# Performance work log

Hardware: AMD Instinct MI355X
Metric: run time of the kernel (lower is better)

## Reference

```python
import jax, jax.numpy as jnp
import numpy as np

NEG = 0.2  # LeakyReLU slope

def lrelu(x):
    return jnp.where(x >= 0, x, NEG * x)

def conv2d(x, w, pad):
    return jax.lax.conv_general_dilated(x, w, (1, 1), [(pad, pad), (pad, pad)],
                                        dimension_numbers=('NCHW', 'OIHW', 'NCHW'))

def maxpool2(x):
    return jax.lax.reduce_window(x, -jnp.inf, jax.lax.max, (1, 1, 2, 2), (1, 1, 2, 2), 'VALID')

def batchnorm(x, g, b, eps=1e-5):
    m = jnp.mean(x, axis=(0, 2, 3), keepdims=True)
    v = jnp.var(x, axis=(0, 2, 3), keepdims=True)
    return (x - m) / jnp.sqrt(v + eps) * g[None, :, None, None] + b[None, :, None, None]

def features(x, cw1, bg1, bb1, cw2, bg2, bb2, cw3, bg3, bb3, cw4, bg4, bb4):
    x = maxpool2(lrelu(batchnorm(conv2d(x, cw1, 1), bg1, bb1)))
    x = maxpool2(lrelu(batchnorm(conv2d(x, cw2, 1), bg2, bb2)))
    x = lrelu(batchnorm(conv2d(x, cw3, 1), bg3, bb3))
    x = lrelu(batchnorm(conv2d(x, cw4, 1), bg4, bb4))
    return x  # [B,64,16,16]

def mhsa(x, wq, bq, wk, bk, wv, bv, rel_h, rel_w, ln_g, ln_b, heads=4):
    B, C, W, H = x.shape
    d, hw = C // heads, W * H
    def proj(w, b):
        return (jnp.einsum('oc,bchw->bohw', w, x) + b[None, :, None, None]).reshape(B, heads, d, hw)
    q, k, v = proj(wq, bq), proj(wk, bk), proj(wv, bv)
    cc = jnp.einsum('bhdi,bhdj->bhij', q, k)                 # content-content
    pos = (rel_h + rel_w).reshape(heads, d, hw)              # relative position bias
    cp = jnp.einsum('hdi,bhdj->bhij', pos, q)                # content-position
    attn = jax.nn.softmax(cc + cp, axis=-1)
    out = jnp.einsum('bhdj,bhij->bhdi', v, attn).reshape(B, C, W, H)
    m = jnp.mean(out, axis=(1, 2, 3), keepdims=True)
    va = jnp.var(out, axis=(1, 2, 3), keepdims=True)
    out = (out - m) / jnp.sqrt(va + 1e-5) * ln_g[None] + ln_b[None]
    return out + x

def cbam(x, cw1, cb1, cw2, cb2, sw, sb):
    avg, mx = jnp.mean(x, axis=(2, 3)), jnp.max(x, axis=(2, 3))
    def exc(f):
        return jnp.einsum('oc,bc->bo', cw2, jax.nn.relu(jnp.einsum('oc,bc->bo', cw1, f) + cb1)) + cb2
    x = jax.nn.sigmoid(exc(avg) + exc(mx))[:, :, None, None] * x
    sf = jnp.stack([jnp.mean(x, axis=1), jnp.max(x, axis=1)], axis=1)  # [B,2,H,W]
    sa = jax.nn.sigmoid(conv2d(sf, sw, 3) + sb[None, :, None, None])
    return sa * x

def sa_module(x, mh, cb):
    return mhsa(x, *mh) + cbam(x, *cb) + x

def setup_inputs() -> dict:
    key = jax.random.key(0)
    ks = jax.random.split(key, 24)
    rn = lambda k, s, sc=1.0: jax.random.normal(k, s, dtype=jnp.float32) * sc
    inp = {
        'input1': rn(ks[0], (64, 1, 64, 64)),
        'input2': rn(ks[1], (5, 5, 1, 64, 64)),
        'conv1_w': rn(ks[2], (64, 1, 3, 3), 0.3),
        'bn1_g': jnp.ones(64), 'bn1_b': jnp.zeros(64),
        'conv2_w': rn(ks[3], (64, 64, 3, 3), 0.05),
        'bn2_g': jnp.ones(64), 'bn2_b': jnp.zeros(64),
        'conv3_w': rn(ks[4], (64, 64, 3, 3), 0.05),
        'bn3_g': jnp.ones(64), 'bn3_b': jnp.zeros(64),
        'conv4_w': rn(ks[5], (64, 64, 3, 3), 0.05),
        'bn4_g': jnp.ones(64), 'bn4_b': jnp.zeros(64),
        'wq': rn(ks[6], (64, 64), 0.12), 'bq': rn(ks[7], (64,), 0.01),
        'wk': rn(ks[8], (64, 64), 0.12), 'bk': rn(ks[9], (64,), 0.01),
        'wv': rn(ks[10], (64, 64), 0.12), 'bv': rn(ks[11], (64,), 0.01),
        'rel_h': rn(ks[12], (1, 4, 16, 1, 16)),
        'rel_w': rn(ks[13], (1, 4, 16, 16, 1)),
        'ln_g': jnp.ones((64, 16, 16)), 'ln_b': jnp.zeros((64, 16, 16)),
        'ca_w1': rn(ks[14], (4, 64), 0.15), 'ca_b1': jnp.zeros(4),
        'ca_w2': rn(ks[15], (64, 4), 0.15), 'ca_b2': jnp.zeros(64),
        'sa_w': rn(ks[16], (1, 2, 7, 7), 0.1), 'sa_b': jnp.zeros(1),
        'cls_w': rn(ks[17], (256,), 0.05),
    }
    return inp

def reference(input1, input2, conv1_w, bn1_g, bn1_b, conv2_w, bn2_g, bn2_b,
              conv3_w, bn3_g, bn3_b, conv4_w, bn4_g, bn4_b,
              wq, bq, wk, bk, wv, bv, rel_h, rel_w, ln_g, ln_b,
              ca_w1, ca_b1, ca_w2, ca_b2, sa_w, sa_b, cls_w):
    fa = (conv1_w, bn1_g, bn1_b, conv2_w, bn2_g, bn2_b, conv3_w, bn3_g, bn3_b, conv4_w, bn4_g, bn4_b)
    mh = (wq, bq, wk, bk, wv, bv, rel_h, rel_w, ln_g, ln_b)
    cb = (ca_w1, ca_b1, ca_w2, ca_b2, sa_w, sa_b)
    q = sa_module(features(input1, *fa), mh, cb)                      # [B,64,16,16]
    S = jax.vmap(lambda imgs: sa_module(features(imgs, *fa), mh, cb))(input2)  # [ncls,shot,64,16,16]
    ncls, shot = input2.shape[0], input2.shape[1]
    B, C, Hh, Ww = q.shape
    hw = Hh * Ww
    # per-class covariance over channels (CovaBlock.cal_covariance)
    X = S.transpose(0, 2, 1, 3, 4).reshape(ncls, C, shot * hw)
    Xc = X - jnp.mean(X, axis=2, keepdims=True)
    cov = jnp.einsum('ncm,ndm->ncd', Xc, Xc) / (hw * shot - 1)        # [ncls,C,C]
    # query similarity: diag(q^T Cov q) done as fused quadratic form
    Q = q.reshape(B, C, hw)
    Qn = Q / jnp.linalg.norm(Q, axis=2, keepdims=True)
    sim = jnp.einsum('bci,jcd,bdi->bji', Qn, cov, Qn)                 # [B,ncls,hw]
    # classifier: LeakyReLU -> Dropout(eval=identity) -> Conv1d(k=hw, stride=hw, no bias)
    out = jnp.einsum('bjk,k->bj', lrelu(sim), cls_w)
    return out
```

## Files before the change

### kernel.cpp

```cpp
#include <hip/hip_runtime.h>
#include <hip/hip_bf16.h>

__device__ __forceinline__ float lrelu(float x){ return x >= 0.f ? x : 0.2f*x; }
__device__ __forceinline__ float sigm(float x){ return 1.f/(1.f+__expf(-x)); }

typedef short short8 __attribute__((ext_vector_type(8)));
typedef float f32x16 __attribute__((ext_vector_type(16)));

static constexpr size_t OFF_X0    = 0;
static constexpr size_t OFF_POS   = 475712;
static constexpr size_t OFF_WQT   = 492096;
static constexpr size_t OFF_STATS = 504384;
static constexpr size_t OFF_P1    = 507456;
static constexpr size_t OFF_P2    = 6340160;
static constexpr size_t OFF_RES   = 10714688;
static constexpr size_t OFF_MU    = 12172864;
static constexpr size_t OFF_COV   = 12173184;
static constexpr size_t OFF_SIM   = 12193664;
static constexpr size_t OFF_R1    = 12275584;
static constexpr size_t OFF_C2    = OFF_R1;
static constexpr size_t OFF_ATP   = OFF_R1;
static constexpr size_t OFF_C3    = OFF_R1 + 5832704;
static constexpr size_t OFF_C4    = OFF_R1 + 8749056;
static constexpr size_t OFF_CKV   = OFF_R1 + 10207232;
static constexpr size_t OFF_MHRAW = OFF_R1 + 14581760;
static constexpr size_t OFF_QN    = OFF_R1 + 17543680;
static constexpr size_t OFF_WH    = OFF_R1 + 21737984;
static constexpr size_t OFF_WL    = OFF_WH + 18432;

__device__ __forceinline__ int bn_group(int img){ return (img < 64) ? 0 : (1 + (img-64)/5); }

__device__ __forceinline__ void bn_ab(const float* __restrict__ sums, int g, int c, float n,
                                      float gw, float bw, float& a, float& b)
{
    const float sum = sums[(g*64+c)*2], ss = sums[(g*64+c)*2+1];
    const float m = sum/n;
    const float var = fmaxf(ss/n - m*m, 0.f);
    const float istd = 1.f/sqrtf(var + 1e-5f);
    a = gw*istd;
    b = bw - m*a;
}

__global__ __launch_bounds__(256) void prep_k(const float* __restrict__ in1, const float* __restrict__ in2,
        const float* __restrict__ relh, const float* __restrict__ relw,
        const float* __restrict__ wq, const float* __restrict__ wk, const float* __restrict__ wv,
        const float* __restrict__ cw2,
        float* __restrict__ ws)
{
    int idx = blockIdx.x*256 + threadIdx.x;
    if (idx < 364544) { ws[OFF_X0+idx] = (idx < 262144 ? in1[idx] : in2[idx-262144]); return; }
    idx -= 364544;
    if (idx < 16384) {
        const int h = idx>>12, r = idx&4095, i = r>>4, d = r&15;
        ws[OFF_POS+idx] = relh[h*256 + d*16 + (i&15)] + relw[h*256 + d*16 + (i>>4)];
        return;
    }
    idx -= 16384;
    if (idx < 12288) {
        const int s = idx/4096, r = idx%4096, c = r>>6, o = r&63;
        const float* wp = (s==0)?wq:((s==1)?wk:wv);
        ws[OFF_WQT+idx] = wp[o*64 + c];
        return;
    }
    idx -= 12288;
    if (idx < 3072) { ws[OFF_STATS+idx] = 0.f; return; }
    idx -= 3072;
    if (idx < 20480) { ws[OFF_COV+idx] = 0.f; return; }
    idx -= 20480;
    if (idx < 36864) {
        const int och = idx/576, r = idx%576, cin = r/9, k9 = r%9;
        const float v = cw2[idx];
        __hip_bfloat16 hb = __float2bfloat16(v);
        const float hv = __bfloat162float(hb);
        __hip_bfloat16 lb = __float2bfloat16(v - hv);
        unsigned short* WH = (unsigned short*)(ws + OFF_WH);
        unsigned short* WL = (unsigned short*)(ws + OFF_WL);
        const int d = k9*4096 + och*64 + cin;
        WH[d] = *(unsigned short*)&hb;
        WL[d] = *(unsigned short*)&lb;
    }
}

template<int H, int W, int CIN, int CH, int OCB, int PT, bool STORE, bool INBN>
__global__ __launch_bounds__(256) void conv3x3_k(const float* __restrict__ in,
                                                 const float* __restrict__ wt,
                                                 float* __restrict__ out,
                                                 float* __restrict__ bnsum,
                                                 const float* __restrict__ isums,
                                                 const float* __restrict__ igw,
                                                 const float* __restrict__ ibw,
                                                 int ihw)
{
    constexpr int P = W + 1;
    constexpr int PLANE = H * P;
    constexpr int HW = H * W;
    constexpr int PASSES = HW / (256 * PT);
    constexpr int NLD = CH * HW / 256;
    __shared__ float lds[CH * PLANE];
    __shared__ float redS[OCB*4], redQ[OCB*4];
    __shared__ float abA[64], abB[64];
    const int img = blockIdx.x;
    const int och0 = blockIdx.y * OCB;
    const int t = threadIdx.x;

    if constexpr (INBN) {
        if (t < CIN) {
            const int gi = bn_group(img);
            const float nin = (float)(((gi==0)?64:5) * ihw);
            float a, b;
            bn_ab(isums, gi, t, nin, igw[t], ibw[t], a, b);
            abA[t]=a; abB[t]=b;
        }
        __syncthreads();
    }

    float acc[PASSES][OCB][PT];
#pragma unroll
    for (int a=0;a<PASSES;a++)
#pragma unroll
      for (int o=0;o<OCB;o++)
#pragma unroll
        for (int p=0;p<PT;p++) acc[a][o][p]=0.f;

    for (int idx = t; idx < CH*HW; idx += 256) {
        const int c = idx / HW, p = idx % HW;
        float v = in[((size_t)img*CIN + c)*HW + p];
        if constexpr (INBN) v = lrelu(abA[c]*v + abB[c]);
        lds[c*PLANE + (p/W)*P + (p%W)] = v;
    }
    __syncthreads();

    for (int cc0 = 0; cc0 < CIN; cc0 += CH) {
        float pre[(CIN > CH) ? NLD : 1];
        if constexpr (CIN > CH) {
            if (cc0 + CH < CIN) {
#pragma unroll
                for (int j=0;j<NLD;j++){
                    const int idx = j*256 + t;
                    const int c = idx / HW, p = idx % HW;
                    pre[j] = in[((size_t)img*CIN + cc0 + CH + c)*HW + p];
                }
            }
        }
        for (int c = 0; c < CH; ++c) {
            float wr[OCB][9];
#pragma unroll
            for (int o=0;o<OCB;o++)
#pragma unroll
              for (int k=0;k<9;k++)
                wr[o][k] = wt[((size_t)(och0+o)*CIN + (cc0+c))*9 + k];
            const float* Lc = lds + c*PLANE;
#pragma unroll
            for (int ps=0; ps<PASSES; ++ps) {
                const int px0 = (ps*256 + t)*PT;
                const int y = px0 / W, x0 = px0 % W;
#pragma unroll
                for (int ky=0; ky<3; ++ky) {
                    const int yy = y + ky - 1;
                    if (yy >= 0 && yy < H) {
                        const float* Lr = Lc + yy*P;
                        float r[PT+2];
                        r[0] = (x0 > 0) ? Lr[x0-1] : 0.f;
#pragma unroll
                        for (int k2=0;k2<PT;k2++) r[k2+1] = Lr[x0+k2];
                        r[PT+1] = (x0+PT < W) ? Lr[x0+PT] : 0.f;
#pragma unroll
                        for (int p=0;p<PT;p++)
#pragma unroll
                          for (int kx=0;kx<3;kx++) {
                              const float v = r[p+kx];
#pragma unroll
                              for (int o=0;o<OCB;o++)
                                  acc[ps][o][p] += v * wr[o][ky*3+kx];
                          }
                    }
                }
            }
        }
        if constexpr (CIN > CH) {
            if (cc0 + CH < CIN) {
                __syncthreads();
#pragma unroll
                for (int j=0;j<NLD;j++){
                    const int idx = j*256 + t;
                    const int c = idx / HW, p = idx % HW;
                    float v = pre[j];
                    if constexpr (INBN) v = lrelu(abA[cc0+CH+c]*v + abB[cc0+CH+c]);
                    lds[c*PLANE + (p/W)*P + (p%W)] = v;
                }
                __syncthreads();
            }
        }
    }
    if constexpr (STORE) {
#pragma unroll
        for (int ps=0; ps<PASSES; ++ps) {
            const int px0 = (ps*256 + t)*PT;
#pragma unroll
            for (int o=0;o<OCB;o++)
#pragma unroll
              for (int p=0;p<PT;p++)
                out[((size_t)img*64 + och0+o)*HW + px0 + p] = acc[ps][o][p];
        }
    }
    const int g = bn_group(img);
    const int wv = t >> 6;
#pragma unroll
    for (int o=0;o<OCB;o++){
        float s=0.f, ss=0.f;
#pragma unroll
        for (int ps=0;ps<PASSES;ps++)
#pragma unroll
          for (int p=0;p<PT;p++){ const float v=acc[ps][o][p]; s+=v; ss+=v*v; }
#pragma unroll
        for (int off=32; off>0; off>>=1){ s += __shfl_xor(s, off); ss += __shfl_xor(ss, off); }
        if ((t&63)==0){ redS[o*4+wv]=s; redQ[o*4+wv]=ss; }
    }
    __syncthreads();
    if (t < OCB*2){
        const int o = t>>1, metric = t&1;
        const float v = metric ? (redQ[o*4]+redQ[o*4+1]+redQ[o*4+2]+redQ[o*4+3])
                               : (redS[o*4]+redS[o*4+1]+redS[o*4+2]+redS[o*4+3]);
        atomicAdd(&bnsum[(g*64 + och0+o)*2 + metric], v);
    }
}

__global__ __launch_bounds__(256) void conv2mfma_k(const float* __restrict__ p1,
        const unsigned short* __restrict__ whi, const unsigned short* __restrict__ wlo,
        float* __restrict__ c2)
{
    __shared__ __align__(16) unsigned short Bx[6*34*72];
    const int img = blockIdx.x, rowblk = blockIdx.y;
    const int t = threadIdx.x;

    for (int i=t; i<6*2*72; i+=256){
        const int ly = i/144, r2 = i%144, xs = r2/72, c = r2%72;
        Bx[(ly*34 + xs*33)*72 + c] = 0;
    }
    unsigned int lo_pack[24];
    const int y0 = rowblk*4 - 1;
    {
        int it = 0;
        for (int lin=t; lin<12288; lin+=256, ++it){
            const int c = lin/192, r = lin%192, ly = r>>5, x = r&31;
            const int y = y0 + ly;
            float v = 0.f;
            if (y>=0 && y<32) v = p1[((size_t)img*64 + c)*1024 + y*32 + x];
            __hip_bfloat16 hb = __float2bfloat16(v);
            const float hv = __bfloat162float(hb);
            __hip_bfloat16 lb = __float2bfloat16(v - hv);
            Bx[(ly*34 + x + 1)*72 + c] = *(unsigned short*)&hb;
            const unsigned int lu = *(unsigned short*)&lb;
            if (it & 1) lo_pack[it>>1] |= (lu<<16); else lo_pack[it>>1] = lu;
        }
    }
    __syncthreads();

    const int lane = t & 63, wv = t >> 6;
    const int mt = wv & 1, ntp = wv >> 1;
    const int m = lane & 31, kg = lane >> 5;
    const int nt0 = ntp*2, nt1 = nt0 + 1;

    f32x16 acc0, acc1;
#pragma unroll
    for (int r=0;r<16;r++){ acc0[r]=0.f; acc1[r]=0.f; }

    for (int ky=0; ky<3; ky++){
      for (int kx=0; kx<3; kx++){
        const int s = ky*3 + kx;
        const unsigned short* wh = whi + ((s*64 + mt*32 + m)<<6) + kg*8;
        const unsigned short* wl = wlo + ((s*64 + mt*32 + m)<<6) + kg*8;
        const int b0 = ((nt0+ky)*34 + m + kx)*72 + kg*8;
        const int b1 = ((nt1+ky)*34 + m + kx)*72 + kg*8;
        short8 ah[4], al[4], bh0[4], bh1[4];
#pragma unroll
        for (int ch=0; ch<4; ch++){
            ah[ch]  = *(const short8*)(wh + ch*16);
            al[ch]  = *(const short8*)(wl + ch*16);
            bh0[ch] = *(const short8*)(Bx + b0 + ch*16);
            bh1[ch] = *(const short8*)(Bx + b1 + ch*16);
        }
#pragma unroll
        for (int ch=0; ch<4; ch++){
            acc0 = __builtin_amdgcn_mfma_f32_32x32x16_bf16(ah[ch], bh0[ch], acc0, 0,0,0);
            acc1 = __builtin_amdgcn_mfma_f32_32x32x16_bf16(ah[ch], bh1[ch], acc1, 0,0,0);
        }
#pragma unroll
        for (int ch=0; ch<4; ch++){
            acc0 = __builtin_amdgcn_mfma_f32_32x32x16_bf16(al[ch], bh0[ch], acc0, 0,0,0);
            acc1 = __builtin_amdgcn_mfma_f32_32x32x16_bf16(al[ch], bh1[ch], acc1, 0,0,0);
        }
      }
    }
    __syncthreads();
    {
        int it = 0;
        for (int lin=t; lin<12288; lin+=256, ++it){
            const int c = lin/192, r = lin%192, ly = r>>5, x = r&31;
            const unsigned int lu = (it&1) ? (lo_pack[it>>1]>>16) : (lo_pack[it>>1]&0xffffu);
            Bx[(ly*34 + x + 1)*72 + c] = (unsigned short)lu;
        }
    }
    __syncthreads();
    for (int ky=0; ky<3; ky++){
      for (int kx=0; kx<3; kx++){
        const int s = ky*3 + kx;
        const unsigned short* wh = whi + ((s*64 + mt*32 + m)<<6) + kg*8;
        const int b0 = ((nt0+ky)*34 + m + kx)*72 + kg*8;
        const int b1 = ((nt1+ky)*34 + m + kx)*72 + kg*8;
#pragma unroll
        for (int ch=0; ch<4; ch++){
            const short8 ah  = *(const short8*)(wh + ch*16);
            const short8 bl0 = *(const short8*)(Bx + b0 + ch*16);
            const short8 bl1 = *(const short8*)(Bx + b1 + ch*16);
            acc0 = __builtin_amdgcn_mfma_f32_32x32x16_bf16(ah, bl0, acc0, 0,0,0);
            acc1 = __builtin_amdgcn_mfma_f32_32x32x16_bf16(ah, bl1, acc1, 0,0,0);
        }
      }
    }
    const int px0 = (rowblk*4 + nt0)*32 + m;
    const int px1 = (rowblk*4 + nt1)*32 + m;
#pragma unroll
    for (int r=0; r<16; r++){
        const int och = mt*32 + (r&3) + 8*(r>>2) + 4*kg;
        c2[((size_t)img*64 + och)*1024 + px0] = acc0[r];
        c2[((size_t)img*64 + och)*1024 + px1] = acc1[r];
    }
}

__global__ __launch_bounds__(256) void bnstats2_k(const float* __restrict__ in, float* __restrict__ sums)
{
    __shared__ float rs[4], rq[4];
    const int img = blockIdx.x, c = blockIdx.y, t = threadIdx.x;
    const float4 v = ((const float4*)(in + ((size_t)img*64 + c)*1024))[t];
    float s = v.x+v.y+v.z+v.w;
    float q = v.x*v.x+v.y*v.y+v.z*v.z+v.w*v.w;
#pragma unroll
    for (int off=32; off>0; off>>=1){ s += __shfl_xor(s, off); q += __shfl_xor(q, off); }
    if ((t&63)==0){ rs[t>>6]=s; rq[t>>6]=q; }
    __syncthreads();
    if (t==0){
        const int g = bn_group(img);
        atomicAdd(&sums[(g*64+c)*2],   rs[0]+rs[1]+rs[2]+rs[3]);
        atomicAdd(&sums[(g*64+c)*2+1], rq[0]+rq[1]+rq[2]+rq[3]);
    }
}

__global__ __launch_bounds__(256) void bnpoolconv1_k(const float* __restrict__ x0,
        const float* __restrict__ cw, const float* __restrict__ sums,
        const float* __restrict__ gw, const float* __restrict__ bw,
        float* __restrict__ out)
{
    __shared__ float xl[64*65];
    const int img = blockIdx.x, och = blockIdx.y, t = threadIdx.x;
    const float* xp = x0 + (size_t)img*4096;
    for (int idx=t; idx<4096; idx+=256) xl[(idx>>6)*65 + (idx&63)] = xp[idx];
    float w[9];
#pragma unroll
    for (int k=0;k<9;k++) w[k] = cw[och*9+k];
    const int g = bn_group(img);
    const float n = (float)(((g==0)?64:5) * 4096);
    float a, b;
    bn_ab(sums, g, och, n, gw[och], bw[och], a, b);
    __syncthreads();
    const int oy = t>>3, ox0 = (t&7)*4;
    float r[4][10];
#pragma unroll
    for (int rr=0; rr<4; ++rr){
        const int yy = 2*oy-1+rr;
#pragma unroll
        for (int cc=0; cc<10; ++cc){
            const int xx = 2*ox0-1+cc;
            r[rr][cc] = (yy>=0 && yy<64 && xx>=0 && xx<64) ? xl[yy*65+xx] : 0.f;
        }
    }
    float4 res;
    float* rp = (float*)&res;
#pragma unroll
    for (int p=0;p<4;p++){
        float best = -1e30f;
#pragma unroll
        for (int sy=0; sy<2; ++sy)
#pragma unroll
          for (int sx=0; sx<2; ++sx){
            float s=0.f;
#pragma unroll
            for (int ky=0;ky<3;ky++)
#pragma unroll
              for (int kx=0;kx<3;kx++)
                s += r[sy+ky][2*p+sx+kx]*w[ky*3+kx];
            best = fmaxf(best, lrelu(a*s+b));
          }
        rp[p] = best;
    }
    *(float4*)(out + ((size_t)img*64+och)*1024 + oy*32 + ox0) = res;
}

template<int H, int W>
__global__ __launch_bounds__(256) void bnpool_k(const float* __restrict__ in, const float* __restrict__ sums,
                                 const float* __restrict__ gw, const float* __restrict__ bw,
                                 float* __restrict__ out)
{
    const int img = blockIdx.x, c = blockIdx.y, t = threadIdx.x;
    const int g = bn_group(img);
    const float n = (float)(((g==0)?64:5) * H * W);
    float a, b;
    bn_ab(sums, g, c, n, gw[c], bw[c], a, b);
    constexpr int W2=W/2, HW=H*W, N2=(H/2)*W2;
    const float* pl = in + ((size_t)img*64 + c)*HW;
    float* po = out + ((size_t)img*64 + c)*N2;
    for (int opx=t; opx<N2; opx+=256) {
        const int oy=opx/W2, ox=opx%W2;
        const float* q = pl + (2*oy)*W + 2*ox;
        const float v0=lrelu(a*q[0]+b), v1=lrelu(a*q[1]+b), v2=lrelu(a*q[W]+b), v3=lrelu(a*q[W+1]+b);
        po[opx] = fmaxf(fmaxf(v0,v1),fmaxf(v2,v3));
    }
}

__global__ __launch_bounds__(256) void proj_k(const float* __restrict__ c4, const float* __restrict__ wT,
               const float* __restrict__ bq, const float* __restrict__ bk, const float* __restrict__ bv,
               const float* __restrict__ sums4, const float* __restrict__ gw4, const float* __restrict__ bw4,
               float* __restrict__ ckv)
{
    __shared__ float xl[64*256];
    const int img = blockIdx.x, s = blockIdx.y, t = threadIdx.x;
    const int gi = bn_group(img);
    const float nin = (float)(((gi==0)?64:5) * 256);
    {
        const float4* in4 = (const float4*)(c4 + (size_t)img*16384);
        float4* xl4 = (float4*)xl;
        for (int i=t; i<4096; i+=256){
            float4 v = in4[i];
            const int c = i>>6;
            float a, b;
            bn_ab(sums4, gi, c, nin, gw4[c], bw4[c], a, b);
            v.x=lrelu(a*v.x+b); v.y=lrelu(a*v.y+b); v.z=lrelu(a*v.z+b); v.w=lrelu(a*v.w+b);
            xl4[i] = v;
        }
    }
    const float* bias = (s==0)?bq:((s==1)?bk:bv);
    const int sofs = (s==0)?16:((s==1)?0:32);
    const float* wp = wT + s*4096;
    const int o0 = (t>>4)*4, i0 = (t&15)*16;
    const int h = o0>>4, d0 = o0&15;
    __syncthreads();
    float acc[4][16];
    float b0[4];
#pragma unroll
    for (int o=0;o<4;o++) b0[o]=bias[o0+o];
#pragma unroll
    for (int o=0;o<4;o++)
#pragma unroll
      for (int i=0;i<16;i++) acc[o][i]=b0[o];
    for (int c=0;c<64;c++){
        const float4 w4 = *(const float4*)(wp + c*64 + o0);
        const float* xr = xl + c*256 + i0;
#pragma unroll
        for (int k=0;k<4;k++){
            const float4 x4 = *(const float4*)(xr + 4*k);
            acc[0][4*k+0]+=w4.x*x4.x; acc[0][4*k+1]+=w4.x*x4.y; acc[0][4*k+2]+=w4.x*x4.z; acc[0][4*k+3]+=w4.x*x4.w;
            acc[1][4*k+0]+=w4.y*x4.x; acc[1][4*k+1]+=w4.y*x4.y; acc[1][4*k+2]+=w4.y*x4.z; acc[1][4*k+3]+=w4.y*x4.w;
            acc[2][4*k+0]+=w4.z*x4.x; acc[2][4*k+1]+=w4.z*x4.y; acc[2][4*k+2]+=w4.z*x4.z; acc[2][4*k+3]+=w4.z*x4.w;
            acc[3][4*k+0]+=w4.w*x4.x; acc[3][4*k+1]+=w4.w*x4.y; acc[3][4*k+2]+=w4.w*x4.z; acc[3][4*k+3]+=w4.w*x4.w;
        }
    }
#pragma unroll
    for (int ii=0;ii<16;ii++){
        const float4 v = make_float4(acc[0][ii],acc[1][ii],acc[2][ii],acc[3][ii]);
        *(float4*)(ckv + (((size_t)img*4 + h)*256 + i0+ii)*48 + sofs + d0) = v;
    }
}

__global__ __launch_bounds__(256) void attnp_k(const float* __restrict__ ckv, const float* __restrict__ pos,
                               float* __restrict__ part)
{
    const int img = blockIdx.x, h = blockIdx.y, jc = blockIdx.z, i = threadIdx.x;
    const size_t jb = (((size_t)img*4 + h)*256)*48;
    float areg[32];
    {
        const float* myrow = ckv + jb + (size_t)i*48;
#pragma unroll
        for (int k=0;k<4;k++) *(float4*)&areg[4*k]    = *(const float4*)(myrow + 16 + 4*k);
#pragma unroll
        for (int k=0;k<4;k++) *(float4*)&areg[16+4*k] = *(const float4*)(pos + h*4096 + i*16 + 4*k);
    }
    float mrun = -1e30f, l = 0.f;
    float accv[16];
#pragma unroll
    for (int d=0;d<16;d++) accv[d]=0.f;

    const int jend = jc*64 + 64;
    for (int j0=jc*64; j0<jend; j0+=2){
        const float* r0 = ckv + jb + (size_t)j0*48;
        const float* r1 = r0 + 48;
        float s0a=0.f, s0b=0.f, s1a=0.f, s1b=0.f;
#pragma unroll
        for (int dd=0; dd<16; ++dd){
            s0a += areg[2*dd]  *r0[2*dd];
            s0b += areg[2*dd+1]*r0[2*dd+1];
            s1a += areg[2*dd]  *r1[2*dd];
            s1b += areg[2*dd+1]*r1[2*dd+1];
        }
        const float s0 = s0a+s0b, s1 = s1a+s1b;
        const float mnew = fmaxf(mrun, fmaxf(s0,s1));
        const float al = __expf(mrun - mnew);
        const float e0 = __expf(s0 - mnew), e1 = __expf(s1 - mnew);
        mrun = mnew;
        l = l*al + e0 + e1;
        const float* v0 = r0 + 32;
        const float* v1 = r1 + 32;
#pragma unroll
        for (int d=0;d<16;d++) accv[d] = accv[d]*al + e0*v0[d] + e1*v1[d];
    }
    float* pp = part + ((((size_t)img*4 + h)*4 + jc)*18)*256;
    pp[i]       = mrun;
    pp[256 + i] = l;
#pragma unroll
    for (int d=0;d<16;d++) pp[(2+d)*256 + i] = accv[d];
}

__global__ __launch_bounds__(256) void attnm_k(const float* __restrict__ part, float* __restrict__ mhraw)
{
    const int img = blockIdx.x, h = blockIdx.y, i = threadIdx.x;
    const float* pb = part + (((size_t)img*4 + h)*4*18)*256;
    float mc[4], lc[4];
#pragma unroll
    for (int c=0;c<4;c++){ mc[c] = pb[c*4608 + i]; lc[c] = pb[c*4608 + 256 + i]; }
    const float ms = fmaxf(fmaxf(mc[0],mc[1]), fmaxf(mc[2],mc[3]));
    float wgt[4]; float ls = 0.f;
#pragma unroll
    for (int c=0;c<4;c++){ wgt[c] = __expf(mc[c]-ms); ls += wgt[c]*lc[c]; }
    const float rl = 1.f/ls;
#pragma unroll
    for (int d=0;d<16;d++){
        float v = 0.f;
#pragma unroll
        for (int c=0;c<4;c++) v += wgt[c]*pb[c*4608 + (2+d)*256 + i];
        mhraw[((size_t)img*64 + h*16 + d)*256 + i] = v*rl;
    }
}

__global__ __launch_bounds__(256) void post_k(const float* __restrict__ mhraw,
        const float* __restrict__ lng, const float* __restrict__ lnb,
        const float* __restrict__ c4,
        const float* __restrict__ sums4, const float* __restrict__ gw4, const float* __restrict__ bw4,
        const float* __restrict__ w1, const float* __restrict__ b1,
        const float* __restrict__ w2, const float* __restrict__ b2,
        const float* __restrict__ sw, const float* __restrict__ sb,
        float* __restrict__ res)
{
    __shared__ float r1[256], r2[256];
    __shared__ float favg[64], fmx[64], z1s[8], ca[64];
    __shared__ float sf[512];
    __shared__ float wl[98];
    __shared__ float mh_s[2];
    __shared__ float aA[64], aB[64];
    __shared__ float sa_l[256];
    const int img = blockIdx.x, t = threadIdx.x;
    const float* mb  = mhraw + (size_t)img*16384;
    const float* fbr = c4    + (size_t)img*16384;

    if (t<64){
        const int gi = bn_group(img);
        const float nin = (float)(((gi==0)?64:5) * 256);
        float a, b;
        bn_ab(sums4, gi, t, nin, gw4[t], bw4[t], a, b);
        aA[t]=a; aB[t]=b;
    }
    if (t<98) wl[t] = sw[t];

    {
        const float4* mb4 = (const float4*)mb;
        float s=0.f, ss=0.f;
        for (int i=t; i<4096; i+=256){
            const float4 v = mb4[i];
            s  += v.x+v.y+v.z+v.w;
            ss += v.x*v.x+v.y*v.y+v.z*v.z+v.w*v.w;
        }
        r1[t]=s; r2[t]=ss; __syncthreads();
        for (int st=128;st>0;st>>=1){ if(t<st){r1[t]+=r1[t+st]; r2[t]+=r2[t+st];} __syncthreads(); }
        if (t==0){
            const float m = r1[0]/16384.f;
            const float var = fmaxf(r2[0]/16384.f - m*m, 0.f);
            mh_s[0]=m; mh_s[1]=1.f/sqrtf(var+1e-5f);
        }
    }
    {
        const int c = t>>2, part = t&3;
        const float a = aA[c], b = aB[c];
        const float4* p4 = (const float4*)(fbr + c*256 + part*64);
        float s=0.f, mx=-1e30f;
        for (int k=0;k<16;k++){
            const float4 v = p4[k];
            const float f0=lrelu(a*v.x+b), f1=lrelu(a*v.y+b), f2=lrelu(a*v.z+b), f3=lrelu(a*v.w+b);
            s += f0+f1+f2+f3;
            mx = fmaxf(mx, fmaxf(fmaxf(f0,f1),fmaxf(f2,f3)));
        }
        __syncthreads();
        r1[t]=s; r2[t]=mx;
        __syncthreads();
        if (t<64){
            favg[t] = (r1[t*4]+r1[t*4+1]+r1[t*4+2]+r1[t*4+3])/256.f;
            fmx[t]  = fmaxf(fmaxf(r2[t*4],r2[t*4+1]),fmaxf(r2[t*4+2],r2[t*4+3]));
        }
    }
    __syncthreads();
    if (t<8){
        const int which = t>>2, o = t&3;
        const float* f = which? fmx : favg;
        float z = b1[o];
        for (int c=0;c<64;c++) z += w1[o*64+c]*f[c];
        z1s[t] = fmaxf(z, 0.f);
    }
    __syncthreads();
    if (t<64){
        float z = 2.f*b2[t];
#pragma unroll
        for (int k=0;k<4;k++) z += w2[t*4+k]*(z1s[k]+z1s[4+k]);
        ca[t] = sigm(z);
    }
    __syncthreads();
    {
        float s=0.f, mx=-1e30f;
        for (int c=0;c<64;c++){
            const float fv = lrelu(aA[c]*fbr[c*256+t] + aB[c]);
            const float v = ca[c]*fv;
            s += v; mx = fmaxf(mx, v);
        }
        sf[t]     = s/64.f;
        sf[256+t] = mx;
    }
    __syncthreads();
    {
        float sacc = sb[0];
        const int y = t>>4, x = t&15;
        for (int ch=0; ch<2; ++ch)
          for (int ky=0; ky<7; ++ky){
            const int yy = y+ky-3;
            if (yy<0||yy>=16) continue;
            for (int kx=0; kx<7; ++kx){
                const int xx = x+kx-3;
                if (xx<0||xx>=16) continue;
                sacc += sf[ch*256 + yy*16 + xx]*wl[ch*49 + ky*7 + kx];
            }
          }
        sa_l[t] = sigm(sacc);
    }
    __syncthreads();
    {
        const int q = t & 63;
        const int cb = t >> 6;
        const float m = mh_s[0], istd = mh_s[1];
        const float4* mb4 = (const float4*)mb;
        const float4* fb4 = (const float4*)fbr;
        const float4* lg4 = (const float4*)lng;
        const float4* lb4 = (const float4*)lnb;
        float4* res4 = (float4*)(res + (size_t)img*16384);
        const float sa0=sa_l[4*q], sa1=sa_l[4*q+1], sa2=sa_l[4*q+2], sa3=sa_l[4*q+3];
#pragma unroll 4
        for (int cc=0; cc<16; ++cc){
            const int c = cb*16 + cc;
            const int i4 = c*64 + q;
            const float4 mv = mb4[i4], fv = fb4[i4], gv = lg4[i4], bv = lb4[i4];
            const float a = aA[c], b = aB[c], cf = ca[c];
            float4 r;
            r.x = (mv.x-m)*istd*gv.x + bv.x + lrelu(a*fv.x+b)*(2.f + sa0*cf);
            r.y = (mv.y-m)*istd*gv.y + bv.y + lrelu(a*fv.y+b)*(2.f + sa1*cf);
            r.z = (mv.z-m)*istd*gv.z + bv.z + lrelu(a*fv.z+b)*(2.f + sa2*cf);
            r.w = (mv.w-m)*istd*gv.w + bv.w + lrelu(a*fv.w+b)*(2.f + sa3*cf);
            res4[i4] = r;
        }
    }
}

__global__ __launch_bounds__(256) void covmu_k(const float* __restrict__ res, float* __restrict__ mu)
{
    __shared__ float r1[256];
    const int n = blockIdx.x, c = blockIdx.y, t = threadIdx.x;
    float s=0.f;
    for (int sh=0; sh<5; ++sh)
        s += res[((size_t)(64 + n*5 + sh)*64 + c)*256 + t];
    r1[t]=s; __syncthreads();
    for (int st=128;st>0;st>>=1){ if(t<st) r1[t]+=r1[t+st]; __syncthreads(); }
    if (t==0) mu[n*64+c] = r1[0]/1280.f;
}

__global__ __launch_bounds__(256) void cov_k(const float* __restrict__ res, const float* __restrict__ mu,
                                             float* __restrict__ cov)
{
    __shared__ float Xl[64*129];
    const int n = blockIdx.x, by = blockIdx.y, sh = blockIdx.z, t = threadIdx.x;
    const int c = by*16 + (t>>4);
    const int d0 = (t&15)*4;
    float acc[4] = {0.f,0.f,0.f,0.f};
    for (int half=0; half<2; ++half){
        __syncthreads();
        for (int idx=t; idx<8192; idx+=256){
            const int ch = idx>>7, p = idx&127;
            Xl[ch*129+p] = res[((size_t)(64+n*5+sh)*64 + ch)*256 + half*128 + p] - mu[n*64+ch];
        }
        __syncthreads();
        for (int p=0;p<128;p++){
            const float xc = Xl[c*129+p];
#pragma unroll
            for (int k=0;k<4;k++) acc[k] += xc*Xl[(d0+k)*129+p];
        }
    }
#pragma unroll
    for (int k=0;k<4;k++) atomicAdd(&cov[((size_t)n*64 + c)*64 + d0+k], acc[k]*(1.f/1279.f));
}

__global__ __launch_bounds__(64) void qn_k(const float* __restrict__ res, float* __restrict__ qn)
{
    const int b = blockIdx.x, c = blockIdx.y, t = threadIdx.x;
    const size_t base = ((size_t)b*64 + c)*256;
    const float4 v = *(const float4*)(res + base + t*4);
    float ss = v.x*v.x + v.y*v.y + v.z*v.z + v.w*v.w;
#pragma unroll
    for (int off=32; off>0; off>>=1) ss += __shfl_xor(ss, off);
    const float inv = 1.f/sqrtf(ss);
    float4 o; o.x=v.x*inv; o.y=v.y*inv; o.z=v.z*inv; o.w=v.w*inv;
    *(float4*)(qn + base + t*4) = o;
}

__global__ __launch_bounds__(256) void sim_k(const float* __restrict__ qn, const float* __restrict__ cov,
                                             float* __restrict__ sim)
{
    __shared__ float covj[64*65];
    __shared__ float Vl[64*68];
    __shared__ float simred[320];
    const int b = blockIdx.x, iq = blockIdx.y, t = threadIdx.x;
    const int i0g = iq*64;
    for (int idx=t; idx<4096; idx+=256){
        const int c = idx>>6, il = idx&63;
        Vl[c*68+il] = qn[((size_t)b*64+c)*256 + i0g + il];
    }
    for (int idx=t; idx<320; idx+=256) simred[idx]=0.f;
    const int c0 = (t>>4)*4, i0 = (t&15)*4;
    for (int j=0;j<5;j++){
        __syncthreads();
        for (int idx=t; idx<4096; idx+=256)
            covj[(idx>>6)*65 + (idx&63)] = cov[(size_t)j*4096 + idx];
        __syncthreads();
        float pt[4][4];
#pragma unroll
        for (int a=0;a<4;a++)
#pragma unroll
          for (int bb=0;bb<4;bb++) pt[a][bb]=0.f;
        for (int d=0; d<64; ++d){
            const float4 vv = *(const float4*)&Vl[d*68 + i0];
            float cw[4];
#pragma unroll
            for (int cc=0;cc<4;cc++) cw[cc] = covj[(c0+cc)*65 + d];
#pragma unroll
            for (int cc=0;cc<4;cc++){
                pt[cc][0] += cw[cc]*vv.x;
                pt[cc][1] += cw[cc]*vv.y;
                pt[cc][2] += cw[cc]*vv.z;
                pt[cc][3] += cw[cc]*vv.w;
            }
        }
#pragma unroll
        for (int ii=0;ii<4;ii++){
            float s = 0.f;
#pragma unroll
            for (int cc=0;cc<4;cc++) s += pt[cc][ii]*Vl[(c0+cc)*68 + i0+ii];
            atomicAdd(&simred[j*64 + i0 + ii], s);
        }
    }
    __syncthreads();
    for (int idx=t; idx<320; idx+=256){
        const int j = idx>>6, il = idx&63;
        sim[((size_t)b*5 + j)*256 + i0g + il] = simred[idx];
    }
}

__global__ __launch_bounds__(256) void cls_k(const float* __restrict__ sim, const float* __restrict__ cw,
                                             float* __restrict__ out)
{
    __shared__ float red[256];
    const int b = blockIdx.x, t = threadIdx.x;
    const float w = cw[t];
    for (int j=0;j<5;j++){
        const float v = sim[((size_t)b*5 + j)*256 + t];
        red[t] = lrelu(v)*w;
        __syncthreads();
        for (int st=128;st>0;st>>=1){ if(t<st) red[t]+=red[t+st]; __syncthreads(); }
        if (t==0) out[b*5+j] = red[0];
        __syncthreads();
    }
}

extern "C" void kernel_launch(void* const* d_in, const int* in_sizes, int n_in,
                              void* d_out, int out_size, void* d_ws, size_t ws_size,
                              hipStream_t stream)
{
    const float* IN[31];
    for (int i=0;i<31;i++) IN[i] = (const float*)d_in[i];
    float* W = (float*)d_ws;
    float* OUT = (float*)d_out;
    const unsigned short* WHp = (const unsigned short*)(W + OFF_WH);
    const unsigned short* WLp = (const unsigned short*)(W + OFF_WL);

    prep_k<<<1772,256,0,stream>>>(IN[0],IN[1],IN[20],IN[21],IN[14],IN[16],IN[18],IN[5],W);

    conv3x3_k<64,64,1,1,4,4,false,false><<<dim3(89,16),256,0,stream>>>(W+OFF_X0, IN[2], nullptr, W+OFF_STATS, nullptr,nullptr,nullptr,0);
    bnpoolconv1_k<<<dim3(89,64),256,0,stream>>>(W+OFF_X0, IN[2], W+OFF_STATS, IN[3], IN[4], W+OFF_P1);

    conv2mfma_k<<<dim3(89,8),256,0,stream>>>(W+OFF_P1, WHp, WLp, W+OFF_C2);
    bnstats2_k<<<dim3(89,64),256,0,stream>>>(W+OFF_C2, W+OFF_STATS+768);
    bnpool_k<32,32><<<dim3(89,64),256,0,stream>>>(W+OFF_C2, W+OFF_STATS+768, IN[6], IN[7], W+OFF_P2);

    conv3x3_k<16,16,64,16,8,1,true,false><<<dim3(89,8),256,0,stream>>>(W+OFF_P2, IN[8], W+OFF_C3, W+OFF_STATS+1536, nullptr,nullptr,nullptr,0);

    conv3x3_k<16,16,64,16,8,1,true,true><<<dim3(89,8),256,0,stream>>>(W+OFF_C3, IN[11], W+OFF_C4, W+OFF_STATS+2304,
                                                                      W+OFF_STATS+1536, IN[9], IN[10], 256);

    proj_k<<<dim3(89,3),256,0,stream>>>(W+OFF_C4, W+OFF_WQT, IN[15], IN[17], IN[19],
                                        W+OFF_STATS+2304, IN[12], IN[13], W+OFF_CKV);
    attnp_k<<<dim3(89,4,4),256,0,stream>>>(W+OFF_CKV, W+OFF_POS, W+OFF_ATP);
    attnm_k<<<dim3(89,4),256,0,stream>>>(W+OFF_ATP, W+OFF_MHRAW);

    post_k<<<89,256,0,stream>>>(W+OFF_MHRAW, IN[22], IN[23], W+OFF_C4,
                                W+OFF_STATS+2304, IN[12], IN[13],
                                IN[24], IN[25], IN[26], IN[27], IN[28], IN[29], W+OFF_RES);

    covmu_k<<<dim3(5,64),256,0,stream>>>(W+OFF_RES, W+OFF_MU);
    cov_k<<<dim3(5,4,5),256,0,stream>>>(W+OFF_RES, W+OFF_MU, W+OFF_COV);
    qn_k<<<dim3(64,64),64,0,stream>>>(W+OFF_RES, W+OFF_QN);
    sim_k<<<dim3(64,4),256,0,stream>>>(W+OFF_QN, W+OFF_COV, W+OFF_SIM);
    cls_k<<<64,256,0,stream>>>(W+OFF_SIM, IN[30], OUT);
}
```

Baseline: 530.3 us.

## Emit padded bf16 hi/lo NHWC activations from conv1 and fuse BN stats into conv2

The conv1+BN+pool kernel now writes its output as padded channel-last bf16 hi/lo pairs, with the zero border set in prep, so conv2 no longer converts fp32 to split bf16 in its load loop. Conv2 loads tiles straight into XOR-swizzled LDS and does all three MFMA products (hi*hi, lo*hi, hi*lo) in one pass over smaller 2-row blocks. It also reduces BN statistics from its accumulators, which removes the separate bnstats2 kernel. The costs are a larger workspace region, more atomics, and a prep kernel that does more zeroing.

```diff
diff --git a/kernel.cpp b/kernel.cpp
--- a/kernel.cpp
+++ b/kernel.cpp
@@ -12,7 +12,7 @@
 static constexpr size_t OFF_WQT   = 492096;
 static constexpr size_t OFF_STATS = 504384;
 static constexpr size_t OFF_P1    = 507456;
-static constexpr size_t OFF_P2    = 6340160;
+static constexpr size_t OFF_P2    = 7092224;
 static constexpr size_t OFF_RES   = 10714688;
 static constexpr size_t OFF_MU    = 12172864;
 static constexpr size_t OFF_COV   = 12173184;
@@ -78,6 +78,16 @@
         const int d = k9*4096 + och*64 + cin;
         WH[d] = *(unsigned short*)&hb;
         WL[d] = *(unsigned short*)&lb;
+        return;
+    }
+    idx -= 36864;
+    if (idx < 751872) {
+        const int img = idx/8448, r = idx%8448;
+        const int pos = r>>6, d = r&63;
+        int ypad, xpad;
+        if (pos < 68){ ypad = (pos<34)?0:33; xpad = (pos<34)?pos:(pos-34); }
+        else { const int q = pos-68; ypad = 1 + (q>>1); xpad = (q&1)*33; }
+        ws[OFF_P1 + (((size_t)img*34 + ypad)*34 + xpad)*64 + d] = 0.f;
     }
 }
 
@@ -225,175 +235,134 @@
     }
 }
 
-__global__ __launch_bounds__(256) void conv2mfma_k(const float* __restrict__ p1,
+__global__ __launch_bounds__(256) void bnpoolconv1_k(const float* __restrict__ x0,
+        const float* __restrict__ cw, const float* __restrict__ sums,
+        const float* __restrict__ gw, const float* __restrict__ bw,
+        unsigned short* __restrict__ p1p)
+{
+    __shared__ float xl[10*64];
+    const int img = blockIdx.x, band = blockIdx.y, t = threadIdx.x;
+    const int oy0 = band*4;
+    const float* xp = x0 + (size_t)img*4096;
+    for (int idx=t; idx<640; idx+=256){
+        const int iy = idx>>6, ix = idx&63;
+        const int gy = 2*oy0 - 1 + iy;
+        xl[idx] = (gy>=0 && gy<64) ? xp[gy*64+ix] : 0.f;
+    }
+    const int g = bn_group(img);
+    const float n = (float)(((g==0)?64:5) * 4096);
+    __syncthreads();
+    const int p = t>>1, half = t&1;
+    const int ly = p>>5, ox = p&31;
+    float r[4][4];
+#pragma unroll
+    for (int dy=0;dy<4;dy++){
+        const float* Lr = xl + (2*ly+dy)*64;
+#pragma unroll
+        for (int dx=0;dx<4;dx++){
+            const int xx = 2*ox-1+dx;
+            r[dy][dx] = (xx>=0 && xx<64) ? Lr[xx] : 0.f;
+        }
+    }
+    short8 hv[4], lv[4];
+#pragma unroll
+    for (int o=0;o<32;o++){
+        const int och = half*32 + o;
+        float w[9];
+#pragma unroll
+        for (int k=0;k<9;k++) w[k] = cw[och*9+k];
+        float a, b;
+        bn_ab(sums, g, och, n, gw[och], bw[och], a, b);
+        float best = -1e30f;
+#pragma unroll
+        for (int sy=0;sy<2;sy++)
+#pragma unroll
+          for (int sx=0;sx<2;sx++){
+            float s=0.f;
+#pragma unroll
+            for (int ky=0;ky<3;ky++)
+#pragma unroll
+              for (int kx=0;kx<3;kx++) s += r[sy+ky][sx+kx]*w[ky*3+kx];
+            best = fmaxf(best, lrelu(a*s+b));
+          }
+        __hip_bfloat16 hb = __float2bfloat16(best);
+        const float hf = __bfloat162float(hb);
+        __hip_bfloat16 lb = __float2bfloat16(best - hf);
+        hv[o>>3][o&7] = (short)*(unsigned short*)&hb;
+        lv[o>>3][o&7] = (short)*(unsigned short*)&lb;
+    }
+    const size_t base = ((((size_t)img*34 + (oy0+ly) + 1)*34) + ox + 1)*128 + half*32;
+#pragma unroll
+    for (int j=0;j<4;j++){
+        *(short8*)(p1p + base + j*8)      = hv[j];
+        *(short8*)(p1p + base + 64 + j*8) = lv[j];
+    }
+}
+
+__global__ __launch_bounds__(256,4) void conv2mfma_k(const unsigned short* __restrict__ p1p,
         const unsigned short* __restrict__ whi, const unsigned short* __restrict__ wlo,
-        float* __restrict__ c2)
-{
-    __shared__ __align__(16) unsigned short Bx[6*34*72];
+        float* __restrict__ c2, float* __restrict__ bnsum)
+{
+    __shared__ __align__(16) unsigned short Bx[136*128];
     const int img = blockIdx.x, rowblk = blockIdx.y;
     const int t = threadIdx.x;
-
-    for (int i=t; i<6*2*72; i+=256){
-        const int ly = i/144, r2 = i%144, xs = r2/72, c = r2%72;
-        Bx[(ly*34 + xs*33)*72 + c] = 0;
-    }
-    unsigned int lo_pack[24];
-    const int y0 = rowblk*4 - 1;
     {
-        int it = 0;
-        for (int lin=t; lin<12288; lin+=256, ++it){
-            const int c = lin/192, r = lin%192, ly = r>>5, x = r&31;
-            const int y = y0 + ly;
-            float v = 0.f;
-            if (y>=0 && y<32) v = p1[((size_t)img*64 + c)*1024 + y*32 + x];
-            __hip_bfloat16 hb = __float2bfloat16(v);
-            const float hv = __bfloat162float(hb);
-            __hip_bfloat16 lb = __float2bfloat16(v - hv);
-            Bx[(ly*34 + x + 1)*72 + c] = *(unsigned short*)&hb;
-            const unsigned int lu = *(unsigned short*)&lb;
-            if (it & 1) lo_pack[it>>1] |= (lu<<16); else lo_pack[it>>1] = lu;
-        }
-    }
-    __syncthreads();
-
+        const unsigned short* src = p1p + (((size_t)img*34 + rowblk*2)*34)*128;
+        for (int idx=t; idx<2176; idx+=256){
+            const int pos = idx>>4, sub = idx&15;
+            const short8 v = *(const short8*)(src + pos*128 + sub*8);
+            *(short8*)(Bx + pos*128 + ((sub ^ (pos&7))<<3)) = v;
+        }
+    }
+    __syncthreads();
     const int lane = t & 63, wv = t >> 6;
     const int mt = wv & 1, ntp = wv >> 1;
     const int m = lane & 31, kg = lane >> 5;
-    const int nt0 = ntp*2, nt1 = nt0 + 1;
-
-    f32x16 acc0, acc1;
-#pragma unroll
-    for (int r=0;r<16;r++){ acc0[r]=0.f; acc1[r]=0.f; }
-
+    f32x16 acc;
+#pragma unroll
+    for (int r=0;r<16;r++) acc[r]=0.f;
+
+#pragma unroll
     for (int ky=0; ky<3; ky++){
+#pragma unroll
       for (int kx=0; kx<3; kx++){
         const int s = ky*3 + kx;
         const unsigned short* wh = whi + ((s*64 + mt*32 + m)<<6) + kg*8;
         const unsigned short* wl = wlo + ((s*64 + mt*32 + m)<<6) + kg*8;
-        const int b0 = ((nt0+ky)*34 + m + kx)*72 + kg*8;
-        const int b1 = ((nt1+ky)*34 + m + kx)*72 + kg*8;
-        short8 ah[4], al[4], bh0[4], bh1[4];
+        const int pos = (ntp+ky)*34 + m + kx;
+        const int pb  = pos << 7;
+        const int sw  = (pos & 7) << 3;
 #pragma unroll
         for (int ch=0; ch<4; ch++){
-            ah[ch]  = *(const short8*)(wh + ch*16);
-            al[ch]  = *(const short8*)(wl + ch*16);
-            bh0[ch] = *(const short8*)(Bx + b0 + ch*16);
-            bh1[ch] = *(const short8*)(Bx + b1 + ch*16);
-        }
-#pragma unroll
-        for (int ch=0; ch<4; ch++){
-            acc0 = __builtin_amdgcn_mfma_f32_32x32x16_bf16(ah[ch], bh0[ch], acc0, 0,0,0);
-            acc1 = __builtin_amdgcn_mfma_f32_32x32x16_bf16(ah[ch], bh1[ch], acc1, 0,0,0);
-        }
-#pragma unroll
-        for (int ch=0; ch<4; ch++){
-            acc0 = __builtin_amdgcn_mfma_f32_32x32x16_bf16(al[ch], bh0[ch], acc0, 0,0,0);
-            acc1 = __builtin_amdgcn_mfma_f32_32x32x16_bf16(al[ch], bh1[ch], acc1, 0,0,0);
+            const short8 ah = *(const short8*)(wh + ch*16);
+            const short8 al = *(const short8*)(wl + ch*16);
+            const short8 bh = *(const short8*)(Bx + pb + ((ch*16 + (kg<<3)) ^ sw));
+            const short8 bl = *(const short8*)(Bx + pb + (64 + ((ch*16 + (kg<<3)) ^ sw)));
+            acc = __builtin_amdgcn_mfma_f32_32x32x16_bf16(ah, bh, acc, 0,0,0);
+            acc = __builtin_amdgcn_mfma_f32_32x32x16_bf16(al, bh, acc, 0,0,0);
+            acc = __builtin_amdgcn_mfma_f32_32x32x16_bf16(ah, bl, acc, 0,0,0);
         }
       }
     }
-    __syncthreads();
-    {
-        int it = 0;
-        for (int lin=t; lin<12288; lin+=256, ++it){
-            const int c = lin/192, r = lin%192, ly = r>>5, x = r&31;
-            const unsigned int lu = (it&1) ? (lo_pack[it>>1]>>16) : (lo_pack[it>>1]&0xffffu);
-            Bx[(ly*34 + x + 1)*72 + c] = (unsigned short)lu;
-        }
-    }
-    __syncthreads();
-    for (int ky=0; ky<3; ky++){
-      for (int kx=0; kx<3; kx++){
-        const int s = ky*3 + kx;
-        const unsigned short* wh = whi + ((s*64 + mt*32 + m)<<6) + kg*8;
-        const int b0 = ((nt0+ky)*34 + m + kx)*72 + kg*8;
-        const int b1 = ((nt1+ky)*34 + m + kx)*72 + kg*8;
-#pragma unroll
-        for (int ch=0; ch<4; ch++){
-            const short8 ah  = *(const short8*)(wh + ch*16);
-            const short8 bl0 = *(const short8*)(Bx + b0 + ch*16);
-            const short8 bl1 = *(const short8*)(Bx + b1 + ch*16);
-            acc0 = __builtin_amdgcn_mfma_f32_32x32x16_bf16(ah, bl0, acc0, 0,0,0);
-            acc1 = __builtin_amdgcn_mfma_f32_32x32x16_bf16(ah, bl1, acc1, 0,0,0);
-        }
-      }
-    }
-    const int px0 = (rowblk*4 + nt0)*32 + m;
-    const int px1 = (rowblk*4 + nt1)*32 + m;
+    const int py = rowblk*2 + ntp;
+    float* co = c2 + ((size_t)img*64)*1024 + py*32 + m;
 #pragma unroll
     for (int r=0; r<16; r++){
         const int och = mt*32 + (r&3) + 8*(r>>2) + 4*kg;
-        c2[((size_t)img*64 + och)*1024 + px0] = acc0[r];
-        c2[((size_t)img*64 + och)*1024 + px1] = acc1[r];
-    }
-}
-
-__global__ __launch_bounds__(256) void bnstats2_k(const float* __restrict__ in, float* __restrict__ sums)
-{
-    __shared__ float rs[4], rq[4];
-    const int img = blockIdx.x, c = blockIdx.y, t = threadIdx.x;
-    const float4 v = ((const float4*)(in + ((size_t)img*64 + c)*1024))[t];
-    float s = v.x+v.y+v.z+v.w;
-    float q = v.x*v.x+v.y*v.y+v.z*v.z+v.w*v.w;
-#pragma unroll
-    for (int off=32; off>0; off>>=1){ s += __shfl_xor(s, off); q += __shfl_xor(q, off); }
-    if ((t&63)==0){ rs[t>>6]=s; rq[t>>6]=q; }
-    __syncthreads();
-    if (t==0){
-        const int g = bn_group(img);
-        atomicAdd(&sums[(g*64+c)*2],   rs[0]+rs[1]+rs[2]+rs[3]);
-        atomicAdd(&sums[(g*64+c)*2+1], rq[0]+rq[1]+rq[2]+rq[3]);
-    }
-}
-
-__global__ __launch_bounds__(256) void bnpoolconv1_k(const float* __restrict__ x0,
-        const float* __restrict__ cw, const float* __restrict__ sums,
-        const float* __restrict__ gw, const float* __restrict__ bw,
-        float* __restrict__ out)
-{
-    __shared__ float xl[64*65];
-    const int img = blockIdx.x, och = blockIdx.y, t = threadIdx.x;
-    const float* xp = x0 + (size_t)img*4096;
-    for (int idx=t; idx<4096; idx+=256) xl[(idx>>6)*65 + (idx&63)] = xp[idx];
-    float w[9];
-#pragma unroll
-    for (int k=0;k<9;k++) w[k] = cw[och*9+k];
+        co[(size_t)och*1024] = acc[r];
+    }
     const int g = bn_group(img);
-    const float n = (float)(((g==0)?64:5) * 4096);
-    float a, b;
-    bn_ab(sums, g, och, n, gw[och], bw[och], a, b);
-    __syncthreads();
-    const int oy = t>>3, ox0 = (t&7)*4;
-    float r[4][10];
-#pragma unroll
-    for (int rr=0; rr<4; ++rr){
-        const int yy = 2*oy-1+rr;
-#pragma unroll
-        for (int cc=0; cc<10; ++cc){
-            const int xx = 2*ox0-1+cc;
-            r[rr][cc] = (yy>=0 && yy<64 && xx>=0 && xx<64) ? xl[yy*65+xx] : 0.f;
-        }
-    }
-    float4 res;
-    float* rp = (float*)&res;
-#pragma unroll
-    for (int p=0;p<4;p++){
-        float best = -1e30f;
-#pragma unroll
-        for (int sy=0; sy<2; ++sy)
-#pragma unroll
-          for (int sx=0; sx<2; ++sx){
-            float s=0.f;
-#pragma unroll
-            for (int ky=0;ky<3;ky++)
-#pragma unroll
-              for (int kx=0;kx<3;kx++)
-                s += r[sy+ky][2*p+sx+kx]*w[ky*3+kx];
-            best = fmaxf(best, lrelu(a*s+b));
-          }
-        rp[p] = best;
-    }
-    *(float4*)(out + ((size_t)img*64+och)*1024 + oy*32 + ox0) = res;
+#pragma unroll
+    for (int r=0; r<16; r++){
+        float sv = acc[r], qv = acc[r]*acc[r];
+#pragma unroll
+        for (int off=16; off>0; off>>=1){ sv += __shfl_xor(sv, off); qv += __shfl_xor(qv, off); }
+        if (m == r){
+            const int och = mt*32 + (r&3) + 8*(r>>2) + 4*kg;
+            atomicAdd(&bnsum[(g*64+och)*2],   sv);
+            atomicAdd(&bnsum[(g*64+och)*2+1], qv);
+        }
+    }
 }
 
 template<int H, int W>
@@ -801,14 +770,14 @@
     float* OUT = (float*)d_out;
     const unsigned short* WHp = (const unsigned short*)(W + OFF_WH);
     const unsigned short* WLp = (const unsigned short*)(W + OFF_WL);
-
-    prep_k<<<1772,256,0,stream>>>(IN[0],IN[1],IN[20],IN[21],IN[14],IN[16],IN[18],IN[5],W);
+    unsigned short* P1P = (unsigned short*)(W + OFF_P1);
+
+    prep_k<<<4709,256,0,stream>>>(IN[0],IN[1],IN[20],IN[21],IN[14],IN[16],IN[18],IN[5],W);
 
     conv3x3_k<64,64,1,1,4,4,false,false><<<dim3(89,16),256,0,stream>>>(W+OFF_X0, IN[2], nullptr, W+OFF_STATS, nullptr,nullptr,nullptr,0);
-    bnpoolconv1_k<<<dim3(89,64),256,0,stream>>>(W+OFF_X0, IN[2], W+OFF_STATS, IN[3], IN[4], W+OFF_P1);
-
-    conv2mfma_k<<<dim3(89,8),256,0,stream>>>(W+OFF_P1, WHp, WLp, W+OFF_C2);
-    bnstats2_k<<<dim3(89,64),256,0,stream>>>(W+OFF_C2, W+OFF_STATS+768);
+    bnpoolconv1_k<<<dim3(89,8),256,0,stream>>>(W+OFF_X0, IN[2], W+OFF_STATS, IN[3], IN[4], P1P);
+
+    conv2mfma_k<<<dim3(89,16),256,0,stream>>>(P1P, WHp, WLp, W+OFF_C2, W+OFF_STATS+768);
     bnpool_k<32,32><<<dim3(89,64),256,0,stream>>>(W+OFF_C2, W+OFF_STATS+768, IN[6], IN[7], W+OFF_P2);
 
     conv3x3_k<16,16,64,16,8,1,true,false><<<dim3(89,8),256,0,stream>>>(W+OFF_P2, IN[8], W+OFF_C3, W+OFF_STATS+1536, nullptr,nullptr,nullptr,0);
```

Result: slower. 881.6 us (+66.3%).
